# Performance work log

Hardware: AMD Instinct MI355X
Metric: run time of the kernel (lower is better)

The kernel has to match this reference:

```python
import jax, jax.numpy as jnp
import numpy as np

B, S, C = 4, 2048, 1024
H, D = 16, 64            # num_heads, head_size
N_STATE = H * D          # 1024
WINDOW = 256             # window_size (causal local window)
SCALE_INV = 1.0 / np.sqrt(D).astype(np.float32)  # sqrt_scale_inv**2 = 1/scale


def setup_inputs() -> dict:
    key = jax.random.key(0)
    ks = jax.random.split(key, 5)
    return {
        "x": jax.random.normal(ks[0], (B, S, C), dtype=jnp.float32),
        "W_qkv": jax.random.normal(ks[1], (3 * N_STATE, C), dtype=jnp.float32) * 0.02,
        "b_qkv": jax.random.normal(ks[2], (3 * N_STATE,), dtype=jnp.float32) * 0.02,
        "W_proj": jax.random.normal(ks[3], (C, N_STATE), dtype=jnp.float32) * 0.02,
        "b_proj": jax.random.normal(ks[4], (C,), dtype=jnp.float32) * 0.02,
    }


def reference(x, W_qkv, b_qkv, W_proj, b_proj):
    # fused QKV projection (channel_last Linear: y = x @ W.T + b)
    qkv = jnp.einsum("bsc,nc->bsn", x, W_qkv) + b_qkv        # [B,S,3*n_state]
    q, k, v = jnp.split(qkv, 3, axis=-1)

    def split_heads(t):  # [B,S,H*D] -> [B,H,S,D]
        return t.reshape(B, S, H, D).transpose(0, 2, 1, 3)

    q, k, v = split_heads(q), split_heads(k), split_heads(v)

    # scaled dot scores: matmul then multiply by 1/scale (scale = sqrt(head_size))
    scores = jnp.einsum("bhqd,bhkd->bhqk", q, k) * SCALE_INV  # [B,H,S,S]

    # window_ar mask: key j visible to query i iff 0 <= i - j < WINDOW
    i = jnp.arange(S)[:, None]
    j = jnp.arange(S)[None, :]
    allowed = (j <= i) & (i - j < WINDOW)                     # [S,S]
    scores = jnp.where(allowed, scores, -jnp.inf)

    attn = jax.nn.softmax(scores, axis=-1)                    # [B,H,S,S]
    ctx = jnp.einsum("bhqk,bhkd->bhqd", attn, v)              # [B,H,S,D]
    ctx = ctx.transpose(0, 2, 1, 3).reshape(B, S, N_STATE)    # merge heads

    out = jnp.einsum("bsn,cn->bsc", ctx, W_proj) + b_proj     # [B,S,C]
    return out
```

## Files before the change

kernel.cpp:

```cpp
#include <hip/hip_runtime.h>
#include <stdint.h>

#define S_LEN 2048
#define NH 16
#define HD 64
#define CDIM 1024
#define QKV_LD 3072
#define WIN 256

typedef __attribute__((ext_vector_type(8))) short bf16x8;
typedef __attribute__((ext_vector_type(4))) short bf16x4;
typedef __attribute__((ext_vector_type(4))) float f32x4;

__device__ __forceinline__ short f2bf(float f) {
  uint32_t u = __builtin_bit_cast(uint32_t, f);
  u += 0x7fffu + ((u >> 16) & 1u);
  return (short)(u >> 16);
}

__global__ void cvt_f32_bf16(const float* __restrict__ in, short* __restrict__ out, int n4) {
  int i = blockIdx.x * 256 + threadIdx.x;
  if (i >= n4) return;
  float4 v = ((const float4*)in)[i];
  bf16x4 o;
  o[0] = f2bf(v.x); o[1] = f2bf(v.y); o[2] = f2bf(v.z); o[3] = f2bf(v.w);
  ((bf16x4*)out)[i] = o;
}

__device__ __forceinline__ void gl_lds16(const short* g, short* lds) {
  __builtin_amdgcn_global_load_lds(
      (const __attribute__((address_space(1))) uint32_t*)(uintptr_t)g,
      (__attribute__((address_space(3))) uint32_t*)(uintptr_t)lds,
      16, 0, 0);
}

template <int BF16OUT>
__global__ __launch_bounds__(256) void gemm_bias(
    const short* __restrict__ A, const short* __restrict__ Bt,
    const float* __restrict__ bias, void* __restrict__ Cout,
    int M, int N, int K)
{
  __shared__ __align__(16) short Asm[128 * 32];
  __shared__ __align__(16) short Bsm[128 * 32];
  const int tid = threadIdx.x;
  const int wave = tid >> 6;
  const int lane = tid & 63;
  const int wm = wave >> 1, wn = wave & 1;
  const int m0 = blockIdx.y * 128, n0 = blockIdx.x * 128;

  const int srow = lane >> 2;
  const int scol = (lane & 3) * 8;
  const short* Ag0 = A + (size_t)(m0 + wave * 16 + srow) * K + scol;
  const short* Ag1 = A + (size_t)(m0 + (wave + 4) * 16 + srow) * K + scol;
  const short* Bg0 = Bt + (size_t)(n0 + wave * 16 + srow) * K + scol;
  const short* Bg1 = Bt + (size_t)(n0 + (wave + 4) * 16 + srow) * K + scol;
  short* lA0 = &Asm[wave * 512];
  short* lA1 = &Asm[(wave + 4) * 512];
  short* lB0 = &Bsm[wave * 512];
  short* lB1 = &Bsm[(wave + 4) * 512];

  f32x4 acc[4][4] = {};

  const int frow = lane & 15;
  const int fcol = (lane >> 4) * 8;

  for (int k0 = 0; k0 < K; k0 += 32) {
    gl_lds16(Ag0 + k0, lA0);
    gl_lds16(Ag1 + k0, lA1);
    gl_lds16(Bg0 + k0, lB0);
    gl_lds16(Bg1 + k0, lB1);
    __syncthreads();
    bf16x8 af[4], bfv[4];
#pragma unroll
    for (int i = 0; i < 4; i++) {
      af[i]  = *(const bf16x8*)&Asm[(wm * 64 + i * 16 + frow) * 32 + fcol];
      bfv[i] = *(const bf16x8*)&Bsm[(wn * 64 + i * 16 + frow) * 32 + fcol];
    }
#pragma unroll
    for (int mi = 0; mi < 4; mi++)
#pragma unroll
      for (int ni = 0; ni < 4; ni++)
        acc[mi][ni] = __builtin_amdgcn_mfma_f32_16x16x32_bf16(af[mi], bfv[ni], acc[mi][ni], 0, 0, 0);
    __syncthreads();
  }

  const int erow = (lane >> 4) * 4;
  const int ecol = lane & 15;
#pragma unroll
  for (int ni = 0; ni < 4; ni++) {
    int n = n0 + wn * 64 + ni * 16 + ecol;
    float bs = bias[n];
#pragma unroll
    for (int mi = 0; mi < 4; mi++) {
      int m = m0 + wm * 64 + mi * 16 + erow;
#pragma unroll
      for (int j = 0; j < 4; j++) {
        float v = acc[mi][ni][j] + bs;
        if (BF16OUT)
          ((short*)Cout)[(size_t)(m + j) * N + n] = f2bf(v);
        else
          ((float*)Cout)[(size_t)(m + j) * N + n] = v;
      }
    }
  }
}

__global__ __launch_bounds__(256) void attn_win(
    const short* __restrict__ qkv, short* __restrict__ ctx)
{
  const int tid = threadIdx.x;
  const int wave = tid >> 6, lane = tid & 63;
  const int grp = blockIdx.x % 32;
  const int h = (blockIdx.x / 32) % NH;
  const int b = blockIdx.x / (32 * NH);
  const int qb = (grp * 4 + wave) * 16;

  const int cl = lane & 15;
  const int g  = lane >> 4;

  const size_t rowQ = (size_t)(b * S_LEN + qb + cl) * QKV_LD + h * HD;
  bf16x8 qf0 = *(const bf16x8*)&qkv[rowQ + g * 8];
  bf16x8 qf1 = *(const bf16x8*)&qkv[rowQ + 32 + g * 8];

  float m_run = -1e30f, l_run = 0.f;
  f32x4 acc[4] = {};
  const f32x4 zero = {};

  const int kstart = qb >= WIN ? qb - WIN : 0;
  const int q_glob = qb + cl;

  for (int k0 = kstart; k0 <= qb; k0 += 16) {
    const size_t rowK = (size_t)(b * S_LEN + k0 + cl) * QKV_LD + CDIM + h * HD;
    bf16x8 kf0 = *(const bf16x8*)&qkv[rowK + g * 8];
    bf16x8 kf1 = *(const bf16x8*)&qkv[rowK + 32 + g * 8];
    f32x4 st = __builtin_amdgcn_mfma_f32_16x16x32_bf16(kf0, qf0, zero, 0, 0, 0);
    st = __builtin_amdgcn_mfma_f32_16x16x32_bf16(kf1, qf1, st, 0, 0, 0);

    float s[4]; bool ok[4];
    float mt = -1e30f;
#pragma unroll
    for (int e = 0; e < 4; e++) {
      int key = k0 + 4 * g + e;
      ok[e] = (key <= q_glob) && (q_glob - key < WIN);
      s[e] = st[e] * 0.125f;
      if (ok[e]) mt = fmaxf(mt, s[e]);
    }
    mt = fmaxf(mt, __shfl_xor(mt, 16, 64));
    mt = fmaxf(mt, __shfl_xor(mt, 32, 64));
    float m_new = fmaxf(m_run, mt);
    float scale = __expf(m_run - m_new);
    float p[4]; float ls = 0.f;
#pragma unroll
    for (int e = 0; e < 4; e++) {
      p[e] = ok[e] ? __expf(s[e] - m_new) : 0.f;
      ls += p[e];
    }
    ls += __shfl_xor(ls, 16, 64);
    ls += __shfl_xor(ls, 32, 64);
    l_run = l_run * scale + ls;
    m_run = m_new;
#pragma unroll
    for (int c = 0; c < 4; c++) acc[c] *= scale;

    bf16x4 pf;
#pragma unroll
    for (int e = 0; e < 4; e++) pf[e] = f2bf(p[e]);

    const size_t rowV = (size_t)(b * S_LEN + k0 + 4 * g) * QKV_LD + 2 * CDIM + h * HD + cl;
#pragma unroll
    for (int c = 0; c < 4; c++) {
      bf16x4 vf;
#pragma unroll
      for (int e = 0; e < 4; e++)
        vf[e] = qkv[rowV + (size_t)e * QKV_LD + c * 16];
      acc[c] = __builtin_amdgcn_mfma_f32_16x16x16bf16_1k(vf, pf, acc[c], 0, 0, 0);
    }
  }

  const float inv_l = 1.f / l_run;
  const size_t rowO = (size_t)(b * S_LEN + qb + cl) * CDIM + h * HD;
#pragma unroll
  for (int c = 0; c < 4; c++)
#pragma unroll
    for (int j = 0; j < 4; j++)
      ctx[rowO + c * 16 + 4 * g + j] = f2bf(acc[c][j] * inv_l);
}

extern "C" void kernel_launch(void* const* d_in, const int* in_sizes, int n_in,
                              void* d_out, int out_size, void* d_ws, size_t ws_size,
                              hipStream_t stream) {
  const float* x      = (const float*)d_in[0];
  const float* W_qkv  = (const float*)d_in[1];
  const float* b_qkv  = (const float*)d_in[2];
  const float* W_proj = (const float*)d_in[3];
  const float* b_proj = (const float*)d_in[4];
  float* out = (float*)d_out;

  const int BS = 4 * S_LEN;
  char* ws = (char*)d_ws;
  short* qkv_bf = (short*)ws;
  short* x_bf   = (short*)(ws + (size_t)BS * QKV_LD * 2);
  short* wq_bf  = x_bf + (size_t)BS * CDIM;
  short* wp_bf  = wq_bf + (size_t)QKV_LD * CDIM;
  short* ctx_bf = wp_bf + (size_t)CDIM * CDIM;

  int n4 = BS * CDIM / 4;
  cvt_f32_bf16<<<(n4 + 255) / 256, 256, 0, stream>>>(x, x_bf, n4);
  n4 = QKV_LD * CDIM / 4;
  cvt_f32_bf16<<<(n4 + 255) / 256, 256, 0, stream>>>(W_qkv, wq_bf, n4);
  n4 = CDIM * CDIM / 4;
  cvt_f32_bf16<<<(n4 + 255) / 256, 256, 0, stream>>>(W_proj, wp_bf, n4);

  dim3 g1(QKV_LD / 128, BS / 128);
  gemm_bias<1><<<g1, 256, 0, stream>>>(x_bf, wq_bf, b_qkv, qkv_bf, BS, QKV_LD, CDIM);

  attn_win<<<4 * NH * 32, 256, 0, stream>>>(qkv_bf, ctx_bf);

  dim3 g2(CDIM / 128, BS / 128);
  gemm_bias<0><<<g2, 256, 0, stream>>>(ctx_bf, wp_bf, b_proj, out, BS, CDIM, CDIM);
}
```

Before: 261.1 us.

## Rewrite GEMM as 8-wave 256x128 tile with double-buffered LDS and XOR swizzle

The QKV and output-projection GEMMs move to a 512-thread, 256x128-tile kernel with a 64-wide K step split into two halves. Global-to-LDS loads are double-buffered and prefetched one to two stages ahead under explicit vmcnt waits, and they are interleaved with MFMA phases wrapped in setprio. The LDS layout uses an XOR swizzle to avoid bank conflicts. The aim is to hide memory latency and raise MFMA utilisation, at the cost of more LDS per block, fewer blocks, and a fragile hand-tuned wait/barrier schedule.

```diff
diff --git a/kernel.cpp b/kernel.cpp
--- a/kernel.cpp
+++ b/kernel.cpp
@@ -34,72 +34,108 @@
       16, 0, 0);
 }
 
+#define WAITVM(N) asm volatile("s_waitcnt vmcnt(" #N ")" ::: "memory")
+
 template <int BF16OUT>
-__global__ __launch_bounds__(256) void gemm_bias(
+__global__ __launch_bounds__(512) void gemm8p(
     const short* __restrict__ A, const short* __restrict__ Bt,
     const float* __restrict__ bias, void* __restrict__ Cout,
     int M, int N, int K)
 {
-  __shared__ __align__(16) short Asm[128 * 32];
-  __shared__ __align__(16) short Bsm[128 * 32];
+  __shared__ __align__(16) short Asm[2][2][256 * 32];
+  __shared__ __align__(16) short Bsm[2][2][128 * 32];
   const int tid = threadIdx.x;
-  const int wave = tid >> 6;
-  const int lane = tid & 63;
+  const int wave = tid >> 6, lane = tid & 63;
   const int wm = wave >> 1, wn = wave & 1;
-  const int m0 = blockIdx.y * 128, n0 = blockIdx.x * 128;
-
-  const int srow = lane >> 2;
-  const int scol = (lane & 3) * 8;
-  const short* Ag0 = A + (size_t)(m0 + wave * 16 + srow) * K + scol;
-  const short* Ag1 = A + (size_t)(m0 + (wave + 4) * 16 + srow) * K + scol;
-  const short* Bg0 = Bt + (size_t)(n0 + wave * 16 + srow) * K + scol;
-  const short* Bg1 = Bt + (size_t)(n0 + (wave + 4) * 16 + srow) * K + scol;
-  short* lA0 = &Asm[wave * 512];
-  short* lA1 = &Asm[(wave + 4) * 512];
-  short* lB0 = &Bsm[wave * 512];
-  short* lB1 = &Bsm[(wave + 4) * 512];
+  const int m0 = blockIdx.y * 256, n0 = blockIdx.x * 128;
+  const int cl = lane & 15, g = lane >> 4;
+  const int NT = K >> 6;
+
+  const short* Ab = A + (size_t)m0 * K;
+  const short* Bb = Bt + (size_t)n0 * K;
+
+  const int off0 = tid * 8;
+  const int r0 = off0 >> 5;
+  const int cs0 = ((off0 >> 3) & 3) ^ ((r0 >> 2) & 3);
+  const int off1 = 4096 + tid * 8;
+  const int r1 = off1 >> 5;
+  const int cs1 = ((off1 >> 3) & 3) ^ ((r1 >> 2) & 3);
+  const short* AgL0 = Ab + (size_t)r0 * K + cs0 * 8;
+  const short* AgL1 = Ab + (size_t)r1 * K + cs1 * 8;
+  const short* Bg   = Bb + (size_t)r0 * K + cs0 * 8;
+
+  auto stageA = [&](int t1, int kh) {
+    gl_lds16(AgL0 + t1 * 64 + kh * 32, &Asm[t1 & 1][kh][off0]);
+    gl_lds16(AgL1 + t1 * 64 + kh * 32, &Asm[t1 & 1][kh][off1]);
+  };
+  auto stageB = [&](int t1, int kh) {
+    gl_lds16(Bg + t1 * 64 + kh * 32, &Bsm[t1 & 1][kh][off0]);
+  };
 
   f32x4 acc[4][4] = {};
 
-  const int frow = lane & 15;
-  const int fcol = (lane >> 4) * 8;
-
-  for (int k0 = 0; k0 < K; k0 += 32) {
-    gl_lds16(Ag0 + k0, lA0);
-    gl_lds16(Ag1 + k0, lA1);
-    gl_lds16(Bg0 + k0, lB0);
-    gl_lds16(Bg1 + k0, lB1);
-    __syncthreads();
-    bf16x8 af[4], bfv[4];
-#pragma unroll
-    for (int i = 0; i < 4; i++) {
-      af[i]  = *(const bf16x8*)&Asm[(wm * 64 + i * 16 + frow) * 32 + fcol];
-      bfv[i] = *(const bf16x8*)&Bsm[(wn * 64 + i * 16 + frow) * 32 + fcol];
-    }
-#pragma unroll
-    for (int mi = 0; mi < 4; mi++)
-#pragma unroll
-      for (int ni = 0; ni < 4; ni++)
-        acc[mi][ni] = __builtin_amdgcn_mfma_f32_16x16x32_bf16(af[mi], bfv[ni], acc[mi][ni], 0, 0, 0);
-    __syncthreads();
-  }
-
-  const int erow = (lane >> 4) * 4;
-  const int ecol = lane & 15;
-#pragma unroll
-  for (int ni = 0; ni < 4; ni++) {
-    int n = n0 + wn * 64 + ni * 16 + ecol;
-    float bs = bias[n];
-#pragma unroll
-    for (int mi = 0; mi < 4; mi++) {
-      int m = m0 + wm * 64 + mi * 16 + erow;
-#pragma unroll
-      for (int j = 0; j < 4; j++) {
-        float v = acc[mi][ni][j] + bs;
-        if (BF16OUT)
-          ((short*)Cout)[(size_t)(m + j) * N + n] = f2bf(v);
-        else
-          ((float*)Cout)[(size_t)(m + j) * N + n] = v;
+  stageA(0, 0); stageB(0, 0); stageA(0, 1); stageB(0, 1);
+  stageA(1, 0); stageB(1, 0);
+  WAITVM(3);
+  __builtin_amdgcn_s_barrier();
+
+#define DS_A(MH, KH)                                                          \
+  _Pragma("unroll") for (int i = 0; i < 2; i++) {                             \
+    const int ra = wm * 64 + (MH) * 32 + i * 16 + cl;                         \
+    af[i] = *(const bf16x8*)&Asm[bi][KH][ra * 32 + (((g ^ (ra >> 2)) & 3) * 8)]; \
+  }
+#define DS_B(KH)                                                              \
+  _Pragma("unroll") for (int j = 0; j < 4; j++) {                             \
+    const int rb = wn * 64 + j * 16 + cl;                                     \
+    bfr[j] = *(const bf16x8*)&Bsm[bi][KH][rb * 32 + (((g ^ (rb >> 2)) & 3) * 8)]; \
+  }
+#define MFMA8(MH)                                                             \
+  __builtin_amdgcn_s_barrier();                                               \
+  __builtin_amdgcn_s_setprio(1);                                              \
+  _Pragma("unroll") for (int i = 0; i < 2; i++)                               \
+    _Pragma("unroll") for (int j = 0; j < 4; j++)                             \
+      acc[(MH) * 2 + i][j] = __builtin_amdgcn_mfma_f32_16x16x32_bf16(         \
+          af[i], bfr[j], acc[(MH) * 2 + i][j], 0, 0, 0);                      \
+  __builtin_amdgcn_s_setprio(0);                                              \
+  __builtin_amdgcn_s_barrier();
+
+  for (int t = 0; t < NT; ++t) {
+    const int bi = t & 1;
+    bf16x8 af[2], bfr[4];
+
+    DS_A(0, 0); DS_B(0);
+    if (t + 1 < NT) stageA(t + 1, 1);
+    MFMA8(0);
+
+    DS_A(1, 0);
+    if (t + 1 < NT) stageB(t + 1, 1);
+    MFMA8(1);
+
+    DS_A(0, 1); DS_B(1);
+    if (t + 2 < NT) stageA(t + 2, 0);
+    MFMA8(0);
+
+    DS_A(1, 1);
+    if (t + 2 < NT) stageB(t + 2, 0);
+    if (t + 2 < NT) { WAITVM(3); } else { WAITVM(0); }
+    MFMA8(1);
+  }
+#undef DS_A
+#undef DS_B
+#undef MFMA8
+
+#pragma unroll
+  for (int j = 0; j < 4; j++) {
+    const int n = n0 + wn * 64 + j * 16 + cl;
+    const float bs = bias[n];
+#pragma unroll
+    for (int a = 0; a < 4; a++) {
+      const int mrow = m0 + wm * 64 + (a >> 1) * 32 + (a & 1) * 16 + g * 4;
+#pragma unroll
+      for (int e = 0; e < 4; e++) {
+        const float v = acc[a][j][e] + bs;
+        if (BF16OUT) ((short*)Cout)[(size_t)(mrow + e) * N + n] = f2bf(v);
+        else         ((float*)Cout)[(size_t)(mrow + e) * N + n] = v;
       }
     }
   }
@@ -211,11 +247,11 @@
   n4 = CDIM * CDIM / 4;
   cvt_f32_bf16<<<(n4 + 255) / 256, 256, 0, stream>>>(W_proj, wp_bf, n4);
 
-  dim3 g1(QKV_LD / 128, BS / 128);
-  gemm_bias<1><<<g1, 256, 0, stream>>>(x_bf, wq_bf, b_qkv, qkv_bf, BS, QKV_LD, CDIM);
+  dim3 g1(QKV_LD / 128, BS / 256);
+  gemm8p<1><<<g1, 512, 0, stream>>>(x_bf, wq_bf, b_qkv, qkv_bf, BS, QKV_LD, CDIM);
 
   attn_win<<<4 * NH * 32, 256, 0, stream>>>(qkv_bf, ctx_bf);
 
-  dim3 g2(CDIM / 128, BS / 128);
-  gemm_bias<0><<<g2, 256, 0, stream>>>(ctx_bf, wp_bf, b_proj, out, BS, CDIM, CDIM);
-}
+  dim3 g2(CDIM / 128, BS / 256);
+  gemm8p<0><<<g2, 512, 0, stream>>>(ctx_bf, wp_bf, b_proj, out, BS, CDIM, CDIM);
+}
```

Result: no change. 259.7 us (-0.5%).

## Rewrite GEMMs with 4-stage LDS ring pipeline, XOR swizzle, larger tiles

Applied to the files above, without the earlier changes.

Replaces the single-buffered GEMM with a 512-thread, 128x256-tile kernel that prefetches K-slices three steps ahead into a 4-deep LDS ring and double-buffers register fragments. It uses an XOR swizzle on LDS columns to avoid bank conflicts, remaps workgroups for L2 locality, and raises MFMA issue priority. The goal is to hide global-load latency and the per-iteration full barriers of the old loop. K is now hardcoded to 1024 and N must be a multiple of 256. The manual vmcnt waits and barrier ordering have to stay exactly right, or stages race.

```diff
diff --git a/kernel.cpp b/kernel.cpp
--- a/kernel.cpp
+++ b/kernel.cpp
@@ -34,72 +34,93 @@
       16, 0, 0);
 }
 
+#define WAITVM(N) asm volatile("s_waitcnt vmcnt(" #N ")" ::: "memory")
+
 template <int BF16OUT>
-__global__ __launch_bounds__(256) void gemm_bias(
+__global__ __launch_bounds__(512) void gemm_ring(
     const short* __restrict__ A, const short* __restrict__ Bt,
-    const float* __restrict__ bias, void* __restrict__ Cout,
-    int M, int N, int K)
+    const float* __restrict__ bias, void* __restrict__ Cout, int N)
 {
-  __shared__ __align__(16) short Asm[128 * 32];
-  __shared__ __align__(16) short Bsm[128 * 32];
-  const int tid = threadIdx.x;
-  const int wave = tid >> 6;
-  const int lane = tid & 63;
-  const int wm = wave >> 1, wn = wave & 1;
-  const int m0 = blockIdx.y * 128, n0 = blockIdx.x * 128;
-
-  const int srow = lane >> 2;
-  const int scol = (lane & 3) * 8;
-  const short* Ag0 = A + (size_t)(m0 + wave * 16 + srow) * K + scol;
-  const short* Ag1 = A + (size_t)(m0 + (wave + 4) * 16 + srow) * K + scol;
-  const short* Bg0 = Bt + (size_t)(n0 + wave * 16 + srow) * K + scol;
-  const short* Bg1 = Bt + (size_t)(n0 + (wave + 4) * 16 + srow) * K + scol;
-  short* lA0 = &Asm[wave * 512];
-  short* lA1 = &Asm[(wave + 4) * 512];
-  short* lB0 = &Bsm[wave * 512];
-  short* lB1 = &Bsm[(wave + 4) * 512];
+  constexpr int K = 1024;
+  constexpr int NSUB = 32;
+  __shared__ __align__(16) short Asm[4][128 * 32];
+  __shared__ __align__(16) short Bsm[4][256 * 32];
+  const int tid = threadIdx.x, wave = tid >> 6, lane = tid & 63;
+  const int wm = wave >> 2, wn = wave & 3;
+  const int cl = lane & 15, g = lane >> 4;
+
+  const int gx = gridDim.x;
+  const int nwg = gx * gridDim.y;
+  const int flat = blockIdx.y * gx + blockIdx.x;
+  const int swzb = (flat & 7) * (nwg >> 3) + (flat >> 3);
+  const int m0 = (swzb / gx) * 128;
+  const int n0 = (swzb % gx) * 256;
+
+  const int srow = tid >> 2;
+  const int scol = (((tid & 3) ^ ((tid >> 3) & 3)) << 3);
+  const short* Asrc  = A  + (size_t)(m0 + srow) * K + scol;
+  const short* Bsrc0 = Bt + (size_t)(n0 + srow) * K + scol;
+  const short* Bsrc1 = Bt + (size_t)(n0 + 128 + srow) * K + scol;
+  const int ldso = tid * 8;
+
+  auto stage = [&](int j) {
+    const int st = j & 3;
+    gl_lds16(Asrc  + j * 32, &Asm[st][ldso]);
+    gl_lds16(Bsrc0 + j * 32, &Bsm[st][ldso]);
+    gl_lds16(Bsrc1 + j * 32, &Bsm[st][4096 + ldso]);
+  };
+
+  const int rc = (g ^ ((cl >> 1) & 3)) << 3;
+  const int arow = wm * 64 + cl;
+  const int brow = wn * 64 + cl;
 
   f32x4 acc[4][4] = {};
-
-  const int frow = lane & 15;
-  const int fcol = (lane >> 4) * 8;
-
-  for (int k0 = 0; k0 < K; k0 += 32) {
-    gl_lds16(Ag0 + k0, lA0);
-    gl_lds16(Ag1 + k0, lA1);
-    gl_lds16(Bg0 + k0, lB0);
-    gl_lds16(Bg1 + k0, lB1);
-    __syncthreads();
-    bf16x8 af[4], bfv[4];
+  bf16x8 a0[4], b0[4], a1[4], b1[4];
+
+  stage(0); stage(1); stage(2);
+  WAITVM(3);
+  __builtin_amdgcn_s_barrier();
+
+#define READF(AA, BB, jj) { const int _s = (jj) & 3;                          \
+  _Pragma("unroll") for (int i = 0; i < 4; i++)                               \
+    AA[i] = *(const bf16x8*)&Asm[_s][(arow + i * 16) * 32 + rc];              \
+  _Pragma("unroll") for (int n = 0; n < 4; n++)                               \
+    BB[n] = *(const bf16x8*)&Bsm[_s][(brow + n * 16) * 32 + rc]; }
+
+#define MFMA16(AA, BB)                                                        \
+  __builtin_amdgcn_s_setprio(1);                                              \
+  _Pragma("unroll") for (int i = 0; i < 4; i++)                               \
+    _Pragma("unroll") for (int n = 0; n < 4; n++)                             \
+      acc[i][n] = __builtin_amdgcn_mfma_f32_16x16x32_bf16(AA[i], BB[n], acc[i][n], 0, 0, 0); \
+  __builtin_amdgcn_s_setprio(0);
+
+  READF(a0, b0, 0);
+  for (int j = 0; j < NSUB; j += 2) {
+    READF(a1, b1, j + 1);
+    if (j + 3 < NSUB) { stage(j + 3); WAITVM(3); } else { WAITVM(0); }
+    __builtin_amdgcn_s_barrier();
+    MFMA16(a0, b0);
+
+    if (j + 2 < NSUB) READF(a0, b0, j + 2);
+    if (j + 4 < NSUB) { stage(j + 4); WAITVM(3); } else { WAITVM(0); }
+    __builtin_amdgcn_s_barrier();
+    MFMA16(a1, b1);
+  }
+#undef READF
+#undef MFMA16
+
+#pragma unroll
+  for (int n = 0; n < 4; n++) {
+    const int col = n0 + wn * 64 + n * 16 + cl;
+    const float bs = bias[col];
 #pragma unroll
     for (int i = 0; i < 4; i++) {
-      af[i]  = *(const bf16x8*)&Asm[(wm * 64 + i * 16 + frow) * 32 + fcol];
-      bfv[i] = *(const bf16x8*)&Bsm[(wn * 64 + i * 16 + frow) * 32 + fcol];
-    }
-#pragma unroll
-    for (int mi = 0; mi < 4; mi++)
-#pragma unroll
-      for (int ni = 0; ni < 4; ni++)
-        acc[mi][ni] = __builtin_amdgcn_mfma_f32_16x16x32_bf16(af[mi], bfv[ni], acc[mi][ni], 0, 0, 0);
-    __syncthreads();
-  }
-
-  const int erow = (lane >> 4) * 4;
-  const int ecol = lane & 15;
-#pragma unroll
-  for (int ni = 0; ni < 4; ni++) {
-    int n = n0 + wn * 64 + ni * 16 + ecol;
-    float bs = bias[n];
-#pragma unroll
-    for (int mi = 0; mi < 4; mi++) {
-      int m = m0 + wm * 64 + mi * 16 + erow;
-#pragma unroll
-      for (int j = 0; j < 4; j++) {
-        float v = acc[mi][ni][j] + bs;
-        if (BF16OUT)
-          ((short*)Cout)[(size_t)(m + j) * N + n] = f2bf(v);
-        else
-          ((float*)Cout)[(size_t)(m + j) * N + n] = v;
+      const int row = m0 + wm * 64 + i * 16 + g * 4;
+#pragma unroll
+      for (int e = 0; e < 4; e++) {
+        const float v = acc[i][n][e] + bs;
+        if (BF16OUT) ((short*)Cout)[(size_t)(row + e) * N + col] = f2bf(v);
+        else         ((float*)Cout)[(size_t)(row + e) * N + col] = v;
       }
     }
   }
@@ -211,11 +232,11 @@
   n4 = CDIM * CDIM / 4;
   cvt_f32_bf16<<<(n4 + 255) / 256, 256, 0, stream>>>(W_proj, wp_bf, n4);
 
-  dim3 g1(QKV_LD / 128, BS / 128);
-  gemm_bias<1><<<g1, 256, 0, stream>>>(x_bf, wq_bf, b_qkv, qkv_bf, BS, QKV_LD, CDIM);
+  dim3 g1(QKV_LD / 256, BS / 128);
+  gemm_ring<1><<<g1, 512, 0, stream>>>(x_bf, wq_bf, b_qkv, qkv_bf, QKV_LD);
 
   attn_win<<<4 * NH * 32, 256, 0, stream>>>(qkv_bf, ctx_bf);
 
-  dim3 g2(CDIM / 128, BS / 128);
-  gemm_bias<0><<<g2, 256, 0, stream>>>(ctx_bf, wp_bf, b_proj, out, BS, CDIM, CDIM);
-}
+  dim3 g2(CDIM / 256, BS / 128);
+  gemm_ring<0><<<g2, 512, 0, stream>>>(ctx_bf, wp_bf, b_proj, out, CDIM);
+}
```

After: 249.9 us. 4.3% less time.
